# Kernel optimization log

Hardware: AMD Instinct MI355X
Metric: run time of the kernel (lower is better)

## Reference

```python
import jax, jax.numpy as jnp
import numpy as np

EPS = 1e-5


def setup_inputs() -> dict:
    key = jax.random.key(0)
    ks = jax.random.split(key, 10)
    B, C, H, W = 4, 256, 64, 64
    x = jax.random.normal(ks[0], (B, C, H, W), dtype=jnp.float32)
    s = 1.0 / np.sqrt(C)
    inp = {
        "x": x,
        "gn_w": jnp.ones((C,), jnp.float32),
        "gn_b": jnp.zeros((C,), jnp.float32),
        "wq": jax.random.normal(ks[1], (C, C), jnp.float32) * s,
        "bq": jnp.zeros((C,), jnp.float32),
        "wk": jax.random.normal(ks[2], (C, C), jnp.float32) * s,
        "bk": jnp.zeros((C,), jnp.float32),
        "wv": jax.random.normal(ks[3], (C, C), jnp.float32) * s,
        "bv": jnp.zeros((C,), jnp.float32),
        "wo": jax.random.normal(ks[4], (C, C), jnp.float32) * s,
        "bo": jnp.zeros((C,), jnp.float32),
    }
    return inp


def _forward(x, gn_w, gn_b, wq, bq, wk, bk, wv, bv, wo, bo):
    B, C, H, W = x.shape
    G = C // 2  # num_groups = channels // 2 -> 2 channels per group
    # GroupNorm
    xg = x.reshape(B, G, C // G, H, W)
    mu = jnp.mean(xg, axis=(2, 3, 4), keepdims=True)
    var = jnp.var(xg, axis=(2, 3, 4), keepdims=True)
    hn = ((xg - mu) * jax.lax.rsqrt(var + EPS)).reshape(B, C, H, W)
    hn = hn * gn_w[None, :, None, None] + gn_b[None, :, None, None]
    # tokens: (B, N, C), N = H*W
    h = hn.transpose(0, 2, 3, 1).reshape(B, H * W, C)
    q = h @ wq.T + bq
    k = h @ wk.T + bk
    v = h @ wv.T + bv
    # full NxN attention, scaled by C^-0.5 (as in original)
    scores = jnp.einsum("bnc,bmc->bnm", q, k) * (C ** -0.5)
    attn = jax.nn.softmax(scores, axis=-1)
    h2 = jnp.einsum("bnm,bmc->bnc", attn, v)  # (B, N, C)
    # faithful replication of the original's layout-scrambling reshape:
    # (B,N,C) -> (B,H,W,C) -> permute (B,C,H,W) -> reshape (B,HW,C)
    h2 = h2.reshape(B, H, W, C).transpose(0, 3, 1, 2).reshape(B, H * W, C)
    out = (h2 @ wo.T + bo).reshape(B, C, H, W)
    return x + out


def reference(x, gn_w, gn_b, wq, bq, wk, bk, wv, bv, wo, bo):
    return _forward(x, gn_w, gn_b, wq, bq, wk, bk, wv, bv, wo, bo)
```

## Files before the change

### kernel.cpp

```cpp
#include <hip/hip_runtime.h>

typedef unsigned short u16;
typedef unsigned int   u32;
typedef __attribute__((ext_vector_type(8)))  short short8;
typedef __attribute__((ext_vector_type(4)))  float f32x4;
typedef __attribute__((ext_vector_type(16))) float f32x16;

#define DI __device__ __forceinline__

DI u16 f2bf(float f){
  u32 u = __builtin_bit_cast(u32, f);
  u += 0x7fffu + ((u >> 16) & 1u);
  return (u16)(u >> 16);
}

DI void gl_lds16(const void* g, void* l){
  __builtin_amdgcn_global_load_lds((const __attribute__((address_space(1))) void*)g,
                                   (__attribute__((address_space(3))) void*)l, 16, 0, 0);
}

DI f32x4 mfma16(short8 a, short8 b, f32x4 c){
  return __builtin_amdgcn_mfma_f32_16x16x32_bf16(a, b, c, 0, 0, 0);
}
DI f32x16 mfma32(short8 a, short8 b, f32x16 c){
  return __builtin_amdgcn_mfma_f32_32x32x16_bf16(a, b, c, 0, 0, 0);
}
DI f32x16 z16(){
  f32x16 v;
  #pragma unroll
  for (int i=0;i<16;i++) v[i]=0.f;
  return v;
}

union U8 { u32 u[4]; short8 s; };

#define OFF_WBF   0u
#define OFF_STATS (512u<<10)
#define OFF_Q     ((1u<<20) + (8u<<20))
#define OFF_K     ((1u<<20) + (16u<<20))
#define OFF_VT    ((1u<<20) + (24u<<20))
#define OFF_H2T   OFF_Q
#define OFF_PART  ((1u<<20) + (32u<<20))
#define OFF_ML    ((1u<<20) + (96u<<20))

__global__ void k_prepstats(const float* wq, const float* wk, const float* wv, const float* wo,
                            u16* wbf, const float* x, float2* stats){
  const int bid = blockIdx.x;
  if (bid < 256){
    const int wi = bid >> 6;
    const float* src = (wi==0)?wq:(wi==1)?wk:(wi==2)?wv:wo;
    u16* d = wbf + wi*65536;
    int i = ((bid&63)*256 + threadIdx.x)*4;
    float4 v = *(const float4*)(src + i);
    u32 lo = (u32)f2bf(v.x) | ((u32)f2bf(v.y)<<16);
    u32 hi = (u32)f2bf(v.z) | ((u32)f2bf(v.w)<<16);
    *(uint2*)(d + i) = make_uint2(lo, hi);
    return;
  }
  const int bg = bid - 256;
  const float* p = x + (size_t)bg*8192;
  float s = 0.f, ss = 0.f;
  #pragma unroll
  for (int i=0;i<8;i++){
    float4 v = *(const float4*)(p + threadIdx.x*4 + i*1024);
    s  += v.x+v.y+v.z+v.w;
    ss += v.x*v.x + v.y*v.y + v.z*v.z + v.w*v.w;
  }
  #pragma unroll
  for (int off=1; off<64; off<<=1){ s += __shfl_xor(s, off, 64); ss += __shfl_xor(ss, off, 64); }
  __shared__ float as[4], aq[4];
  int w = threadIdx.x>>6;
  if ((threadIdx.x&63)==0){ as[w]=s; aq[w]=ss; }
  __syncthreads();
  if (threadIdx.x==0){
    s = as[0]+as[1]+as[2]+as[3]; ss = aq[0]+aq[1]+aq[2]+aq[3];
    float mu = s * (1.f/8192.f);
    float var = ss * (1.f/8192.f) - mu*mu;
    stats[bg] = make_float2(mu, rsqrtf(var + 1e-5f));
  }
}

__global__ __launch_bounds__(256,2) void k_qkv(const float* x, const float* gw,
    const float* gb, const float2* stats, const u16* wbf,
    const float* bq, const float* bk, const float* bv,
    u16* qo, u16* ko, u16* vt){
  __shared__ u16 lds_a[64*256];
  const int t = threadIdx.x, row0 = blockIdx.x*64;
  const int w = t>>6, l = t&63, lo = l&15, hi = l>>4;
  {
    const int b = row0>>12, n0 = row0&4095;
    const float* xb = x + (size_t)b*1048576;
    #pragma unroll
    for (int p=0;p<4;p++){
      int c = p*64 + (t>>2);
      float2 st = stats[b*128 + (c>>1)];
      float scl = st.y * gw[c];
      float off = gb[c] - st.x*scl;
      const float* src = xb + (size_t)c*4096 + n0 + (t&3)*16;
      #pragma unroll
      for (int u2=0;u2<4;u2++){
        float4 v = *(const float4*)(src + u2*4);
        float vv[4] = {v.x,v.y,v.z,v.w};
        #pragma unroll
        for (int j=0;j<4;j++){
          int n = (t&3)*16 + u2*4 + j;
          int addr = n*512 + ((c*2) ^ ((n&7)<<4));
          *(u16*)((char*)lds_a + addr) = f2bf(vv[j]*scl + off);
        }
      }
    }
    __syncthreads();
  }
  auto compute = [&](const u16* W, f32x4 acc[4][4]){
    #pragma unroll
    for (int i=0;i<4;i++)
      #pragma unroll
      for (int j=0;j<4;j++) acc[i][j] = (f32x4){0.f,0.f,0.f,0.f};
    const char* Wb = (const char*)W;
    #pragma unroll
    for (int dk=0; dk<4; dk++){
      #pragma unroll
      for (int s=0;s<2;s++){
        short8 af[4], bf[4];
        #pragma unroll
        for (int cf=0;cf<4;cf++){
          int col = w*64 + cf*16 + lo;
          bf[cf] = *(const short8*)(Wb + (size_t)col*512 + dk*128 + s*64 + hi*16);
        }
        #pragma unroll
        for (int rg=0;rg<4;rg++){
          int row = rg*16 + lo;
          af[rg] = *(const short8*)((const char*)lds_a + row*512 + ((dk*128 + s*64 + hi*16) ^ ((row&7)<<4)));
        }
        #pragma unroll
        for (int rg=0;rg<4;rg++)
          #pragma unroll
          for (int cf=0;cf<4;cf++)
            acc[rg][cf] = mfma16(af[rg], bf[cf], acc[rg][cf]);
      }
    }
  };
  f32x4 acc[4][4];
  compute(wbf, acc);
  #pragma unroll
  for (int rg=0;rg<4;rg++)
    #pragma unroll
    for (int cf=0;cf<4;cf++){
      int col = w*64 + cf*16 + lo;
      float bs = bq[col];
      #pragma unroll
      for (int r=0;r<4;r++){
        int grow = row0 + rg*16 + hi*4 + r;
        qo[(size_t)grow*256 + col] = f2bf((acc[rg][cf][r] + bs)*0.09016844f);
      }
    }
  compute(wbf + 65536, acc);
  #pragma unroll
  for (int rg=0;rg<4;rg++)
    #pragma unroll
    for (int cf=0;cf<4;cf++){
      int col = w*64 + cf*16 + lo;
      float bs = bk[col];
      #pragma unroll
      for (int r=0;r<4;r++){
        int grow = row0 + rg*16 + hi*4 + r;
        ko[(size_t)grow*256 + col] = f2bf(acc[rg][cf][r] + bs);
      }
    }
  compute(wbf + 2*65536, acc);
  __syncthreads();
  #pragma unroll
  for (int rg=0;rg<4;rg++)
    #pragma unroll
    for (int cf=0;cf<4;cf++){
      int col = w*64 + cf*16 + lo;
      float bs = bv[col];
      ushort4 pk;
      pk.x = f2bf(acc[rg][cf][0]+bs); pk.y = f2bf(acc[rg][cf][1]+bs);
      pk.z = f2bf(acc[rg][cf][2]+bs); pk.w = f2bf(acc[rg][cf][3]+bs);
      int rl = rg*16 + hi*4;
      int addr = col*128 + ((rl*2) ^ ((col&7)<<4));
      *(ushort4*)((char*)lds_a + addr) = pk;
    }
  __syncthreads();
  {
    int b = row0 >> 12, nb = row0 & 4095;
    #pragma unroll
    for (int p=0;p<8;p++){
      int c = p*32 + (t>>3), i = t&7;
      uint4 vd = *(const uint4*)((const char*)lds_a + c*128 + ((i*16) ^ ((c&7)<<4)));
      *(uint4*)((char*)vt + ((size_t)(b*256 + c)*4096 + nb)*2 + i*16) = vd;
    }
  }
}

__global__ __launch_bounds__(256,2) void k_out(const u16* h2t, const u16* wo,
    const float* bo, const float* x, float* out){
  __shared__ u16 lds_a[64*256];
  const int t = threadIdx.x, row0 = blockIdx.x*64;
  const int w = t>>6, l = t&63, lo = l&15, hi = l>>4;
  {
    const char* Ab = (const char*)h2t + (size_t)row0*512;
    #pragma unroll
    for (int i=0;i<8;i++){
      int row = w*16 + i*2 + (l>>5);
      gl_lds16(Ab + row*512 + (((l&31)*16) ^ ((row&7)<<4)), lds_a + w*4096 + i*512);
    }
    __syncthreads();
  }
  f32x4 acc[4][4];
  #pragma unroll
  for (int i=0;i<4;i++)
    #pragma unroll
    for (int j=0;j<4;j++) acc[i][j] = (f32x4){0.f,0.f,0.f,0.f};
  const char* Wb = (const char*)wo;
  #pragma unroll
  for (int dk=0; dk<4; dk++){
    #pragma unroll
    for (int s=0;s<2;s++){
      short8 af[4], bf[4];
      #pragma unroll
      for (int cf=0;cf<4;cf++){
        int col = w*64 + cf*16 + lo;
        bf[cf] = *(const short8*)(Wb + (size_t)col*512 + dk*128 + s*64 + hi*16);
      }
      #pragma unroll
      for (int rg=0;rg<4;rg++){
        int row = rg*16 + lo;
        af[rg] = *(const short8*)((const char*)lds_a + row*512 + ((dk*128 + s*64 + hi*16) ^ ((row&7)<<4)));
      }
      #pragma unroll
      for (int rg=0;rg<4;rg++)
        #pragma unroll
        for (int cf=0;cf<4;cf++)
          acc[rg][cf] = mfma16(af[rg], bf[cf], acc[rg][cf]);
    }
  }
  #pragma unroll
  for (int rg=0;rg<4;rg++)
    #pragma unroll
    for (int cf=0;cf<4;cf++){
      int col = w*64 + cf*16 + lo;
      float bs = bo[col];
      #pragma unroll
      for (int r=0;r<4;r++){
        size_t flat = (size_t)(row0 + rg*16 + hi*4 + r)*256 + col;
        out[flat] = x[flat] + acc[rg][cf][r] + bs;
      }
    }
}

__global__ __launch_bounds__(512,2) void k_attn(const u16* q, const u16* k,
                                                const u16* vt, u16* part, float2* ml){
  __shared__ char smem[131072];
  const int t = threadIdx.x, w = t>>6, l = t&63;
  const int lq = l&31, h = l>>5;
  const int bid = blockIdx.x;
  const int x = bid&7, idx = bid>>3;
  const int combo = x*2 + (idx&1);
  const int b = combo>>2, ks = combo&3, qt = idx>>1;

  const char* kg = (const char*)k  + ((size_t)b*4096 + (size_t)ks*1024)*512;
  const char* vg = (const char*)vt + (size_t)b*2097152 + (size_t)ks*2048;

  short8 qf[16];
  {
    const char* qrow = (const char*)q + ((size_t)b*4096 + qt*256 + w*32 + lq)*512;
    #pragma unroll
    for (int dk=0;dk<16;dk++) qf[dk] = *(const short8*)(qrow + dk*32 + h*16);
  }

  f32x16 O[8];
  #pragma unroll
  for (int ct=0;ct<8;ct++) O[ct] = z16();
  float m_run = -1e30f, l_run = 0.f;

  auto stage = [&](int ti, int buf){
    #pragma unroll
    for (int sub=0; sub<2; ++sub){
      char* kd = smem + buf*32768 + sub*16384;
      char* vd = smem + 65536 + buf*32768 + sub*16384;
      #pragma unroll
      for (int j=0;j<2;j++){
        int key = w*4 + j*2 + h;
        gl_lds16(kg + (size_t)(ti*64 + sub*32 + key)*512 + (((l&31)*16) ^ ((key&7)<<4)),
                 kd + (w*2+j)*1024);
      }
      #pragma unroll
      for (int j=0;j<2;j++){
        int c = w*32 + j*16 + (l>>2);
        gl_lds16(vg + (size_t)c*8192 + ti*128 + sub*64 + (((l&3)*16) ^ (((l>>3)&3)<<4)),
                 vd + (w*2+j)*1024);
      }
    }
  };

  auto smpv = [&](const f32x16& S, const char* vbuf){
    float pmax = S[0];
    #pragma unroll
    for (int r=1;r<16;r++) pmax = fmaxf(pmax, S[r]);
    pmax = fmaxf(pmax, __shfl_xor(pmax, 32, 64));
    if (__any(pmax > m_run + 8.f)){
      float mn = fmaxf(m_run, pmax);
      float sclq = exp2f(m_run - mn);
      m_run = mn;
      l_run *= sclq;
      #pragma unroll
      for (int r=0;r<16;r++){
        float sr = __shfl(sclq, (r&3)+8*(r>>2)+4*h, 64);
        #pragma unroll
        for (int ct=0;ct<8;ct++) O[ct][r] *= sr;
      }
    }
    float p[16]; float ps = 0.f;
    #pragma unroll
    for (int r=0;r<16;r++){ p[r] = exp2f(S[r] - m_run); ps += p[r]; }
    l_run += ps + __shfl_xor(ps, 32, 64);
    u32 pk[8];
    #pragma unroll
    for (int j=0;j<8;j++){
      u32 u0 = __builtin_bit_cast(u32, p[2*j]);
      u32 u1 = __builtin_bit_cast(u32, p[2*j+1]);
      pk[j] = (u1 & 0xffff0000u) | (u0 >> 16);
    }
    #pragma unroll
    for (int kc=0;kc<2;kc++){
      u32 sA = h ? pk[4*kc]   : pk[4*kc+2];
      u32 sB = h ? pk[4*kc+1] : pk[4*kc+3];
      u32 xA = __shfl_xor(sA, 32, 64);
      u32 xB = __shfl_xor(sB, 32, 64);
      U8 pa;
      pa.u[0] = h ? xA : pk[4*kc];
      pa.u[1] = h ? xB : pk[4*kc+1];
      pa.u[2] = h ? pk[4*kc+2] : xA;
      pa.u[3] = h ? pk[4*kc+3] : xB;
      #pragma unroll
      for (int ct=0;ct<8;ct++){
        short8 vb = *(const short8*)(vbuf + (size_t)(ct*32+lq)*64 + ((kc*32 + h*16) ^ (((lq>>1)&3)<<4)));
        O[ct] = mfma32(pa.s, vb, O[ct]);
      }
    }
  };

  stage(0, 0);
  __syncthreads();

  for (int tile=0; tile<16; ++tile){
    const int cur = tile&1;
    if (tile < 15) stage(tile+1, cur^1);
    const char* kbuf0 = smem + cur*32768;
    const char* kbuf1 = kbuf0 + 16384;
    const char* vbuf0 = smem + 65536 + cur*32768;
    const char* vbuf1 = vbuf0 + 16384;

    f32x16 S0 = z16(), S1 = z16();
    #pragma unroll
    for (int dk=0;dk<16;dk++){
      int dby = (dk*32 + h*16) ^ ((lq&7)<<4);
      short8 k0 = *(const short8*)(kbuf0 + (size_t)lq*512 + dby);
      short8 k1 = *(const short8*)(kbuf1 + (size_t)lq*512 + dby);
      S0 = mfma32(k0, qf[dk], S0);
      S1 = mfma32(k1, qf[dk], S1);
    }

    smpv(S0, vbuf0);
    smpv(S1, vbuf1);
    __syncthreads();
  }

  if (h == 0)
    ml[(size_t)combo*4096 + qt*256 + w*32 + lq] = make_float2(m_run, l_run);
  u16* otile = (u16*)smem;
  char* pbase = (char*)part + ((size_t)combo*4096 + (size_t)qt*256)*512;
  #pragma unroll
  for (int rd=0; rd<2; ++rd){
    __syncthreads();
    if ((w>>2) == rd){
      int wl = w&3;
      #pragma unroll
      for (int ct=0;ct<8;ct++)
        #pragma unroll
        for (int r=0;r<16;r++){
          int row = wl*32 + (r&3) + 8*(r>>2) + 4*h;
          otile[row*256 + ct*32 + lq] = f2bf(O[ct][r]);
        }
    }
    __syncthreads();
    const char* sb2 = (const char*)smem;
    char* gb2 = pbase + (size_t)rd*65536;
    #pragma unroll
    for (int j=0;j<8;j++)
      *(uint4*)(gb2 + t*16 + (size_t)j*8192) = *(const uint4*)(sb2 + t*16 + (size_t)j*8192);
  }
}

__global__ __launch_bounds__(256,2) void k_combine(const u16* part, const float2* ml, u16* h2t){
  __shared__ u16 tile[64*256];
  const int t = threadIdx.x, b = blockIdx.y, n0 = blockIdx.x*64;
  const int n = t>>2, cc = (t&3)*64;
  const int gn = n0 + n;
  float2 st[4]; float ms = -1e30f;
  #pragma unroll
  for (int ksi=0;ksi<4;ksi++){ st[ksi] = ml[(size_t)(b*4+ksi)*4096 + gn]; ms = fmaxf(ms, st[ksi].x); }
  float wn[4]; float denom = 0.f;
  #pragma unroll
  for (int ksi=0;ksi<4;ksi++){ wn[ksi] = exp2f(st[ksi].x - ms); denom += wn[ksi]*st[ksi].y; }
  float inv = 1.f/denom;
  #pragma unroll
  for (int ksi=0;ksi<4;ksi++) wn[ksi] *= inv;
  float acc[64];
  #pragma unroll
  for (int j=0;j<64;j++) acc[j] = 0.f;
  #pragma unroll
  for (int ksi=0;ksi<4;ksi++){
    const u16* src = part + ((size_t)(b*4+ksi)*4096 + gn)*256 + cc;
    float wv = wn[ksi];
    #pragma unroll
    for (int j8=0;j8<8;j8++){
      short8 v = *(const short8*)(src + j8*8);
      #pragma unroll
      for (int e=0;e<8;e++){
        u32 uu = ((u32)(u16)v[e])<<16;
        acc[j8*8+e] += wv * __builtin_bit_cast(float, uu);
      }
    }
  }
  char* tb = (char*)tile;
  #pragma unroll
  for (int j=0;j<32;j++){
    u32 pkv = ((u32)f2bf(acc[2*j+1])<<16) | f2bf(acc[2*j]);
    *(u32*)(tb + n*512 + ((cc*2 + j*4) ^ ((n&7)<<4))) = pkv;
  }
  __syncthreads();
  {
    const char* tbc = (const char*)tile;
    u32 outw[32];
    #pragma unroll
    for (int j=0;j<32;j++){
      u16 v0 = *(const u16*)(tbc + (2*j  )*512 + ((t*2) ^ (((2*j  )&7)<<4)));
      u16 v1 = *(const u16*)(tbc + (2*j+1)*512 + ((t*2) ^ (((2*j+1)&7)<<4)));
      outw[j] = ((u32)v1<<16) | v0;
    }
    char* dst = (char*)h2t + ((size_t)(b*256 + t)*4096 + n0)*2;
    #pragma unroll
    for (int j=0;j<8;j++){
      uint4 vv; vv.x = outw[4*j]; vv.y = outw[4*j+1]; vv.z = outw[4*j+2]; vv.w = outw[4*j+3];
      *(uint4*)(dst + j*16) = vv;
    }
  }
}

extern "C" void kernel_launch(void* const* d_in, const int* in_sizes, int n_in,
                              void* d_out, int out_size, void* d_ws, size_t ws_size,
                              hipStream_t stream) {
  const float* x    = (const float*)d_in[0];
  const float* gn_w = (const float*)d_in[1];
  const float* gn_b = (const float*)d_in[2];
  const float* wq   = (const float*)d_in[3];
  const float* bq   = (const float*)d_in[4];
  const float* wk   = (const float*)d_in[5];
  const float* bk   = (const float*)d_in[6];
  const float* wv   = (const float*)d_in[7];
  const float* bv   = (const float*)d_in[8];
  const float* wo   = (const float*)d_in[9];
  const float* bo   = (const float*)d_in[10];
  float* out = (float*)d_out;
  char* ws = (char*)d_ws;

  u16*    wbf   = (u16*)(ws + OFF_WBF);
  float2* stats = (float2*)(ws + OFF_STATS);
  u16*    qb    = (u16*)(ws + OFF_Q);
  u16*    kb    = (u16*)(ws + OFF_K);
  u16*    vt    = (u16*)(ws + OFF_VT);
  u16*    h2t   = (u16*)(ws + OFF_H2T);
  u16*    part  = (u16*)(ws + OFF_PART);
  float2* ml    = (float2*)(ws + OFF_ML);

  k_prepstats<<<768,        256, 0, stream>>>(wq, wk, wv, wo, wbf, x, stats);
  k_qkv      <<<256,        256, 0, stream>>>(x, gn_w, gn_b, stats, wbf, bq, bk, bv, qb, kb, vt);
  k_attn     <<<256,        512, 0, stream>>>(qb, kb, vt, part, ml);
  k_combine  <<<dim3(64,4), 256, 0, stream>>>(part, ml, h2t);
  k_out      <<<256,        256, 0, stream>>>(h2t, wbf + 3*65536, bo, x, out);
}
```

Before: 161.6 us.

## Halve attention block to 4 waves, single-buffer LDS, double grid size

The attention kernel now runs 256-thread blocks covering 128 query rows instead of 512-thread blocks covering 256, and launches 512 blocks instead of 256. The K/V LDS staging drops from double-buffered 128KB to single-buffered 64KB, so each tile is loaded and then waited on with a barrier instead of being prefetched. The aim is more blocks per CU and better balance across CUs, at the cost of losing load/compute overlap. Each block now reloads the full K/V stream for half as many queries, which doubles K/V traffic.

```diff
diff --git a/kernel.cpp b/kernel.cpp
--- a/kernel.cpp
+++ b/kernel.cpp
@@ -250,9 +250,9 @@
     }
 }
 
-__global__ __launch_bounds__(512,2) void k_attn(const u16* q, const u16* k,
+__global__ __launch_bounds__(256,2) void k_attn(const u16* q, const u16* k,
                                                 const u16* vt, u16* part, float2* ml){
-  __shared__ char smem[131072];
+  __shared__ char smem[65536];
   const int t = threadIdx.x, w = t>>6, l = t&63;
   const int lq = l&31, h = l>>5;
   const int bid = blockIdx.x;
@@ -265,7 +265,7 @@
 
   short8 qf[16];
   {
-    const char* qrow = (const char*)q + ((size_t)b*4096 + qt*256 + w*32 + lq)*512;
+    const char* qrow = (const char*)q + ((size_t)b*4096 + qt*128 + w*32 + lq)*512;
     #pragma unroll
     for (int dk=0;dk<16;dk++) qf[dk] = *(const short8*)(qrow + dk*32 + h*16);
   }
@@ -275,22 +275,22 @@
   for (int ct=0;ct<8;ct++) O[ct] = z16();
   float m_run = -1e30f, l_run = 0.f;
 
-  auto stage = [&](int ti, int buf){
+  auto stage = [&](int ti){
     #pragma unroll
     for (int sub=0; sub<2; ++sub){
-      char* kd = smem + buf*32768 + sub*16384;
-      char* vd = smem + 65536 + buf*32768 + sub*16384;
-      #pragma unroll
-      for (int j=0;j<2;j++){
-        int key = w*4 + j*2 + h;
+      char* kd = smem + sub*16384;
+      char* vd = smem + 32768 + sub*16384;
+      #pragma unroll
+      for (int j=0;j<4;j++){
+        int key = w*8 + j*2 + h;
         gl_lds16(kg + (size_t)(ti*64 + sub*32 + key)*512 + (((l&31)*16) ^ ((key&7)<<4)),
-                 kd + (w*2+j)*1024);
-      }
-      #pragma unroll
-      for (int j=0;j<2;j++){
-        int c = w*32 + j*16 + (l>>2);
+                 kd + (w*4+j)*1024);
+      }
+      #pragma unroll
+      for (int j=0;j<4;j++){
+        int c = w*64 + j*16 + (l>>2);
         gl_lds16(vg + (size_t)c*8192 + ti*128 + sub*64 + (((l&3)*16) ^ (((l>>3)&3)<<4)),
-                 vd + (w*2+j)*1024);
+                 vd + (w*4+j)*1024);
       }
     }
   };
@@ -342,16 +342,13 @@
     }
   };
 
-  stage(0, 0);
-  __syncthreads();
-
   for (int tile=0; tile<16; ++tile){
-    const int cur = tile&1;
-    if (tile < 15) stage(tile+1, cur^1);
-    const char* kbuf0 = smem + cur*32768;
-    const char* kbuf1 = kbuf0 + 16384;
-    const char* vbuf0 = smem + 65536 + cur*32768;
-    const char* vbuf1 = vbuf0 + 16384;
+    stage(tile);
+    __syncthreads();
+    const char* kbuf0 = smem;
+    const char* kbuf1 = smem + 16384;
+    const char* vbuf0 = smem + 32768;
+    const char* vbuf1 = smem + 49152;
 
     f32x16 S0 = z16(), S1 = z16();
     #pragma unroll
@@ -369,28 +366,22 @@
   }
 
   if (h == 0)
-    ml[(size_t)combo*4096 + qt*256 + w*32 + lq] = make_float2(m_run, l_run);
+    ml[(size_t)combo*4096 + qt*128 + w*32 + lq] = make_float2(m_run, l_run);
   u16* otile = (u16*)smem;
-  char* pbase = (char*)part + ((size_t)combo*4096 + (size_t)qt*256)*512;
-  #pragma unroll
-  for (int rd=0; rd<2; ++rd){
-    __syncthreads();
-    if ((w>>2) == rd){
-      int wl = w&3;
-      #pragma unroll
-      for (int ct=0;ct<8;ct++)
-        #pragma unroll
-        for (int r=0;r<16;r++){
-          int row = wl*32 + (r&3) + 8*(r>>2) + 4*h;
-          otile[row*256 + ct*32 + lq] = f2bf(O[ct][r]);
-        }
-    }
-    __syncthreads();
+  #pragma unroll
+  for (int ct=0;ct<8;ct++)
+    #pragma unroll
+    for (int r=0;r<16;r++){
+      int row = w*32 + (r&3) + 8*(r>>2) + 4*h;
+      otile[row*256 + ct*32 + lq] = f2bf(O[ct][r]);
+    }
+  __syncthreads();
+  {
     const char* sb2 = (const char*)smem;
-    char* gb2 = pbase + (size_t)rd*65536;
-    #pragma unroll
-    for (int j=0;j<8;j++)
-      *(uint4*)(gb2 + t*16 + (size_t)j*8192) = *(const uint4*)(sb2 + t*16 + (size_t)j*8192);
+    char* gb2 = (char*)part + ((size_t)combo*4096 + (size_t)qt*128)*512;
+    #pragma unroll
+    for (int j=0;j<16;j++)
+      *(uint4*)(gb2 + t*16 + (size_t)j*4096) = *(const uint4*)(sb2 + t*16 + (size_t)j*4096);
   }
 }
 
@@ -478,7 +469,7 @@
 
   k_prepstats<<<768,        256, 0, stream>>>(wq, wk, wv, wo, wbf, x, stats);
   k_qkv      <<<256,        256, 0, stream>>>(x, gn_w, gn_b, stats, wbf, bq, bk, bv, qb, kb, vt);
-  k_attn     <<<256,        512, 0, stream>>>(qb, kb, vt, part, ml);
+  k_attn     <<<512,        256, 0, stream>>>(qb, kb, vt, part, ml);
   k_combine  <<<dim3(64,4), 256, 0, stream>>>(part, ml, h2t);
   k_out      <<<256,        256, 0, stream>>>(h2t, wbf + 3*65536, bo, x, out);
 }
```

Measured after the change: 163.9 us. No clear change (+1.4%).
